# Performance work log

Hardware: AMD Instinct MI355X
Metric: run time of the kernel (lower is better)

The kernel has to match this reference:

```python
import jax, jax.numpy as jnp
import numpy as np

B = 2048       # batch
D_IN = 512     # input_size
D_MODEL = 1024 # hidden_size / d_model
ED = 2048      # d_inner = 2*d_model
N = 16         # d_state
K = 4          # d_conv
DT = 64        # dt_rank = ceil(d_model/16)
FLAT_H = ED * N
RMS_EPS = 1e-5


def setup_inputs() -> dict:
    key = jax.random.key(0)
    ks = jax.random.split(key, 12)
    rn = lambda k, shape, s: jax.random.normal(k, shape, jnp.float32) * s
    return {
        "x_t": rn(ks[0], (B, D_IN), 1.0),
        "flat_state": rn(ks[1], (B, FLAT_H + ED * (K - 1)), 0.1),
        "W_in_cell": rn(ks[2], (D_MODEL, D_IN), D_IN ** -0.5),
        "norm_w": jnp.ones((D_MODEL,), jnp.float32),
        "W_in": rn(ks[3], (2 * ED, D_MODEL), D_MODEL ** -0.5),
        "conv_w": rn(ks[4], (ED, K), K ** -0.5),  # depthwise conv weight (ED,1,K) squeezed
        "conv_b": rn(ks[5], (ED,), 0.02),
        "W_xproj": rn(ks[6], (DT + 2 * N, ED), ED ** -0.5),
        "W_dt": rn(ks[7], (ED, DT), DT ** -0.5),
        "b_dt": rn(ks[8], (ED,), 0.02),
        "A_log": jnp.log(jnp.broadcast_to(jnp.arange(1, N + 1, dtype=jnp.float32), (ED, N))),
        "D_param": jnp.ones((ED,), jnp.float32),
        "W_out": rn(ks[9], (D_MODEL, ED), ED ** -0.5),
    }


def _rmsnorm(x, w):
    return x * jax.lax.rsqrt(jnp.mean(x * x, axis=-1, keepdims=True) + RMS_EPS) * w


def reference(x_t, flat_state, W_in_cell, norm_w, W_in, conv_w, conv_b,
              W_xproj, W_dt, b_dt, A_log, D_param, W_out):
    # MambaCell.in_proj (bias=False)
    x = x_t @ W_in_cell.T                                  # (B, D_MODEL)
    # unpack flat recurrent state
    h = flat_state[:, :FLAT_H].reshape(B, ED, N)           # SSM state
    inputs = flat_state[:, FLAT_H:].reshape(B, ED, K - 1)  # conv cache

    residual = x
    xn = _rmsnorm(x, norm_w)

    # MambaBlock.step
    xz = xn @ W_in.T                                       # (B, 2*ED)
    x1, z = xz[:, :ED], xz[:, ED:]

    # depthwise causal conv, last output position only
    window = jnp.concatenate([inputs, x1[:, :, None]], axis=2)   # (B, ED, K)
    xc = jnp.einsum("bek,ek->be", window, conv_w) + conv_b
    xs = jax.nn.silu(xc)                                   # (B, ED)

    # selective SSM single step
    dbc = xs @ W_xproj.T                                   # (B, DT+2N)
    delta = jax.nn.softplus(dbc[:, :DT] @ W_dt.T + b_dt)   # (B, ED)
    Bm = dbc[:, DT:DT + N]                                 # (B, N)
    Cm = dbc[:, DT + N:]                                   # (B, N)
    A = -jnp.exp(A_log)                                    # (ED, N)
    dA = jnp.exp(delta[:, :, None] * A[None])              # (B, ED, N)
    dBx = delta[:, :, None] * Bm[:, None, :] * xs[:, :, None]
    h_new = dA * h + dBx                                   # (B, ED, N)
    y = jnp.einsum("ben,bn->be", h_new, Cm) + D_param * xs

    out = (y * jax.nn.silu(z)) @ W_out.T                   # (B, D_MODEL)
    y_t = out + residual                                   # residual connection in ResidualBlock.step

    inputs_new = jnp.concatenate([inputs[:, :, 1:], x1[:, :, None]], axis=2)
    flat_new = jax.lax.stop_gradient(
        jnp.concatenate([h_new.reshape(B, -1), inputs_new.reshape(B, -1)], axis=1))
    return y_t, flat_new
```

## Files before the change

### kernel.cpp

```cpp
#include <hip/hip_runtime.h>
#include <math.h>

#define B 2048
#define D_IN 512
#define D_MODEL 1024
#define ED 2048
#define NSTATE 16
#define KCONV 4
#define DTDIM 64
#define FLAT_H (ED * NSTATE)
#define ROW_STATE (FLAT_H + ED * (KCONV - 1))

typedef __attribute__((ext_vector_type(8))) short short8;
typedef __attribute__((ext_vector_type(4))) short short4v;
typedef __attribute__((ext_vector_type(4))) float f32x4;

__device__ __forceinline__ float sigmoidf_(float x) { return 1.f / (1.f + expf(-x)); }

__device__ __forceinline__ unsigned short f2bf(float f) {
  unsigned u = __float_as_uint(f);
  u += 0x7FFFu + ((u >> 16) & 1u);
  return (unsigned short)(u >> 16);
}
__device__ __forceinline__ float bf2f(unsigned short h) {
  return __uint_as_float((unsigned)h << 16);
}

template <int MODE>
__global__ __launch_bounds__(256) void gemm_nt_mfma(
    const float* __restrict__ A, const float* __restrict__ W,
    float* __restrict__ C, int M, int N, int K, int lda, int ldw, int ldc,
    const float* __restrict__ extra) {
  __shared__ short Ahi[4][128][8];
  __shared__ short Alo[4][128][8];
  __shared__ short Whi[4][128][8];
  __shared__ short Wlo[4][128][8];

  const int tid = threadIdx.x;
  const int lane = tid & 63;
  const int wave = tid >> 6;
  const int wr = wave >> 1;
  const int wc = wave & 1;
  const int m0 = blockIdx.y * 128;
  const int n0 = blockIdx.x * 128;
  const int kg = lane >> 4;
  const int lr = lane & 15;

  f32x4 acc[4][4] = {};

  for (int k0 = 0; k0 < K; k0 += 32) {
#pragma unroll
    for (int it = 0; it < 4; ++it) {
      const int flat = tid + it * 256;
      const int row = flat >> 3;
      const int kq = flat & 7;
      const int tkg = kq >> 1;
      const int j0 = (kq & 1) * 4;
      const float4 av = *(const float4*)(A + (size_t)(m0 + row) * lda + (k0 + kq * 4));
      const float4 wv = *(const float4*)(W + (size_t)(n0 + row) * ldw + (k0 + kq * 4));
      const float af[4] = {av.x, av.y, av.z, av.w};
      const float wf[4] = {wv.x, wv.y, wv.z, wv.w};
      short4v ah, al, wh, wl;
#pragma unroll
      for (int e = 0; e < 4; ++e) {
        const unsigned short h = f2bf(af[e]);
        ah[e] = (short)h;
        al[e] = (short)f2bf(af[e] - bf2f(h));
        const unsigned short hw = f2bf(wf[e]);
        wh[e] = (short)hw;
        wl[e] = (short)f2bf(wf[e] - bf2f(hw));
      }
      *(short4v*)&Ahi[tkg][row][j0] = ah;
      *(short4v*)&Alo[tkg][row][j0] = al;
      *(short4v*)&Whi[tkg][row][j0] = wh;
      *(short4v*)&Wlo[tkg][row][j0] = wl;
    }
    __syncthreads();

    short8 a_h[4], a_l[4], b_h[4], b_l[4];
#pragma unroll
    for (int i = 0; i < 4; ++i) {
      a_h[i] = *(const short8*)&Ahi[kg][wr * 64 + i * 16 + lr][0];
      a_l[i] = *(const short8*)&Alo[kg][wr * 64 + i * 16 + lr][0];
      b_h[i] = *(const short8*)&Whi[kg][wc * 64 + i * 16 + lr][0];
      b_l[i] = *(const short8*)&Wlo[kg][wc * 64 + i * 16 + lr][0];
    }
#pragma unroll
    for (int i = 0; i < 4; ++i)
#pragma unroll
      for (int j = 0; j < 4; ++j) {
        acc[i][j] = __builtin_amdgcn_mfma_f32_16x16x32_bf16(a_h[i], b_h[j], acc[i][j], 0, 0, 0);
        acc[i][j] = __builtin_amdgcn_mfma_f32_16x16x32_bf16(a_l[i], b_h[j], acc[i][j], 0, 0, 0);
        acc[i][j] = __builtin_amdgcn_mfma_f32_16x16x32_bf16(a_h[i], b_l[j], acc[i][j], 0, 0, 0);
      }
    __syncthreads();
  }

#pragma unroll
  for (int i = 0; i < 4; ++i) {
    const int gm = m0 + wr * 64 + i * 16 + kg * 4;
#pragma unroll
    for (int j = 0; j < 4; ++j) {
      const int gn = n0 + wc * 64 + j * 16 + lr;
#pragma unroll
      for (int r = 0; r < 4; ++r) {
        float v = acc[i][j][r];
        if (MODE == 1) {
          v += extra[gn];
          v = (v > 20.f) ? v : log1pf(expf(v));
        } else if (MODE == 2) {
          v += extra[(size_t)(gm + r) * ldc + gn];
        }
        C[(size_t)(gm + r) * ldc + gn] = v;
      }
    }
  }
}

__global__ __launch_bounds__(256) void gemm_nt_splitk(
    const float* __restrict__ A, const float* __restrict__ W,
    float* __restrict__ C, int M, int N, int K, int lda, int ldw, int ldc) {
  __shared__ float As[16][68];
  __shared__ float Ws[16][68];
  const int tid = threadIdx.x;
  const int tx = tid & 15;
  const int ty = tid >> 4;
  const int m0 = blockIdx.y * 64;
  const int n0 = blockIdx.x * 64;
  const int kchunk = K / gridDim.z;
  const int kbeg = blockIdx.z * kchunk;

  float acc[4][4] = {};
  const int lr = tid >> 4;
  const int lc = tid & 15;

  for (int k0 = kbeg; k0 < kbeg + kchunk; k0 += 16) {
#pragma unroll
    for (int i = 0; i < 4; i++) {
      const int r = lr + i * 16;
      const int gk = k0 + lc;
      As[lc][r] = A[(size_t)(m0 + r) * lda + gk];
      const int gn = n0 + r;
      Ws[lc][r] = (gn < N) ? W[(size_t)gn * ldw + gk] : 0.f;
    }
    __syncthreads();
#pragma unroll
    for (int k = 0; k < 16; k++) {
      float a[4], w[4];
#pragma unroll
      for (int i = 0; i < 4; i++) a[i] = As[k][ty * 4 + i];
#pragma unroll
      for (int j = 0; j < 4; j++) w[j] = Ws[k][tx * 4 + j];
#pragma unroll
      for (int i = 0; i < 4; i++)
#pragma unroll
        for (int j = 0; j < 4; j++) acc[i][j] += a[i] * w[j];
    }
    __syncthreads();
  }

#pragma unroll
  for (int i = 0; i < 4; i++) {
    const int gm = m0 + ty * 4 + i;
#pragma unroll
    for (int j = 0; j < 4; j++) {
      const int gn = n0 + tx * 4 + j;
      if (gn >= N) continue;
      atomicAdd(&C[(size_t)gm * ldc + gn], acc[i][j]);
    }
  }
}

__global__ __launch_bounds__(256) void rmsnorm_kernel(
    const float* __restrict__ x, const float* __restrict__ w,
    float* __restrict__ xn) {
  const int b = blockIdx.x;
  const float* xr = x + (size_t)b * D_MODEL;
  float ss = 0.f;
  for (int i = threadIdx.x; i < D_MODEL; i += 256) {
    float v = xr[i];
    ss += v * v;
  }
#pragma unroll
  for (int off = 32; off > 0; off >>= 1) ss += __shfl_down(ss, off, 64);
  __shared__ float red[4];
  if ((threadIdx.x & 63) == 0) red[threadIdx.x >> 6] = ss;
  __syncthreads();
  const float tot = red[0] + red[1] + red[2] + red[3];
  const float scale = rsqrtf(tot * (1.f / (float)D_MODEL) + 1e-5f);
  float* xnr = xn + (size_t)b * D_MODEL;
  for (int i = threadIdx.x; i < D_MODEL; i += 256) xnr[i] = xr[i] * scale * w[i];
}

__global__ __launch_bounds__(256) void conv_silu_kernel(
    const float* __restrict__ flat_state, const float* __restrict__ xz,
    const float* __restrict__ conv_w, const float* __restrict__ conv_b,
    float* __restrict__ xs, float* __restrict__ outFlat) {
  const int id = blockIdx.x * 256 + threadIdx.x;
  const int b = id >> 11;
  const int e = id & (ED - 1);
  const float* inp = flat_state + (size_t)b * ROW_STATE + FLAT_H + e * 3;
  const float i0 = inp[0], i1 = inp[1], i2 = inp[2];
  const float x1 = xz[(size_t)b * (2 * ED) + e];
  const float* cw = conv_w + e * 4;
  const float xc = i0 * cw[0] + i1 * cw[1] + i2 * cw[2] + x1 * cw[3] + conv_b[e];
  xs[(size_t)b * ED + e] = xc * sigmoidf_(xc);
  float* on = outFlat + (size_t)b * ROW_STATE + FLAT_H + e * 3;
  on[0] = i1;
  on[1] = i2;
  on[2] = x1;
}

__global__ __launch_bounds__(256) void state_kernel(
    const float* __restrict__ flat_state, const float* __restrict__ xz,
    const float* __restrict__ xs, const float* __restrict__ dbc,
    const float* __restrict__ delta, const float* __restrict__ A_log,
    const float* __restrict__ D_param, float* __restrict__ outFlat,
    float* __restrict__ yz) {
  const int id = blockIdx.x * 256 + threadIdx.x;
  const int b = id >> 11;
  const int e = id & (ED - 1);
  const float d = delta[(size_t)b * ED + e];
  const float xsv = xs[(size_t)b * ED + e];
  const float* hb = flat_state + (size_t)b * ROW_STATE + e * NSTATE;
  float* ho = outFlat + (size_t)b * ROW_STATE + e * NSTATE;
  const float* dbcb = dbc + (size_t)b * 96;
  const float* al = A_log + e * NSTATE;
  float y = 0.f;
#pragma unroll
  for (int n = 0; n < NSTATE; n++) {
    const float Aen = -expf(al[n]);
    const float dA = expf(d * Aen);
    const float hn = dA * hb[n] + d * dbcb[DTDIM + n] * xsv;
    ho[n] = hn;
    y += hn * dbcb[DTDIM + NSTATE + n];
  }
  y += D_param[e] * xsv;
  const float z = xz[(size_t)b * (2 * ED) + ED + e];
  yz[(size_t)b * ED + e] = y * (z * sigmoidf_(z));
}

extern "C" void kernel_launch(void* const* d_in, const int* in_sizes, int n_in,
                              void* d_out, int out_size, void* d_ws, size_t ws_size,
                              hipStream_t stream) {
  const float* x_t       = (const float*)d_in[0];
  const float* flat_state= (const float*)d_in[1];
  const float* W_in_cell = (const float*)d_in[2];
  const float* norm_w    = (const float*)d_in[3];
  const float* W_in      = (const float*)d_in[4];
  const float* conv_w    = (const float*)d_in[5];
  const float* conv_b    = (const float*)d_in[6];
  const float* W_xproj   = (const float*)d_in[7];
  const float* W_dt      = (const float*)d_in[8];
  const float* b_dt      = (const float*)d_in[9];
  const float* A_log     = (const float*)d_in[10];
  const float* D_param   = (const float*)d_in[11];
  const float* W_out     = (const float*)d_in[12];

  float* y_t_out = (float*)d_out;
  float* outFlat = (float*)d_out + (size_t)B * D_MODEL;

  float* ws = (float*)d_ws;
  float* x     = ws;
  float* xn    = x + (size_t)B * D_MODEL;
  float* xz    = xn + (size_t)B * D_MODEL;
  float* xs    = xz + (size_t)B * 2 * ED;
  float* dbc   = xs + (size_t)B * ED;
  float* delta = dbc + (size_t)B * 96;
  float* yz    = delta + (size_t)B * ED;

  dim3 blk(256);

  hipMemsetAsync(dbc, 0, (size_t)B * 96 * sizeof(float), stream);

  gemm_nt_mfma<0><<<dim3(D_MODEL / 128, B / 128), blk, 0, stream>>>(
      x_t, W_in_cell, x, B, D_MODEL, D_IN, D_IN, D_IN, D_MODEL, nullptr);
  rmsnorm_kernel<<<dim3(B), blk, 0, stream>>>(x, norm_w, xn);
  gemm_nt_mfma<0><<<dim3(2 * ED / 128, B / 128), blk, 0, stream>>>(
      xn, W_in, xz, B, 2 * ED, D_MODEL, D_MODEL, D_MODEL, 2 * ED, nullptr);
  conv_silu_kernel<<<dim3((B * ED) / 256), blk, 0, stream>>>(
      flat_state, xz, conv_w, conv_b, xs, outFlat);
  gemm_nt_splitk<<<dim3(2, B / 64, 4), blk, 0, stream>>>(
      xs, W_xproj, dbc, B, 96, ED, ED, ED, 96);
  gemm_nt_mfma<1><<<dim3(ED / 128, B / 128), blk, 0, stream>>>(
      dbc, W_dt, delta, B, ED, DTDIM, 96, DTDIM, ED, b_dt);
  state_kernel<<<dim3((B * ED) / 256), blk, 0, stream>>>(
      flat_state, xz, xs, dbc, delta, A_log, D_param, outFlat, yz);
  gemm_nt_mfma<2><<<dim3(D_MODEL / 128, B / 128), blk, 0, stream>>>(
      yz, W_out, y_t_out, B, D_MODEL, ED, ED, ED, D_MODEL, x);
}
```

Before: 1.010 ms.

## Coalesce state and conv kernels, precompute -exp(A_log), vectorize rmsnorm

The SSM state update now gives each thread four consecutive state entries, loaded and stored as float4 so the large flat_state read and write are coalesced. Partial y sums are combined with lane shuffles. The -exp(A_log) term is computed once by a small prep kernel instead of per element, and written into the workspace slot of xn, which is dead by then. The conv kernel runs one block per batch row and stages the conv cache in LDS so global reads and writes are coalesced. RMSNorm is vectorized with float4 and the x-projection split-K depth goes from 4 to 8, at the cost of one extra launch and more atomic adds.

```diff
diff --git a/kernel.cpp b/kernel.cpp
--- a/kernel.cpp
+++ b/kernel.cpp
@@ -175,12 +175,9 @@
     const float* __restrict__ x, const float* __restrict__ w,
     float* __restrict__ xn) {
   const int b = blockIdx.x;
-  const float* xr = x + (size_t)b * D_MODEL;
-  float ss = 0.f;
-  for (int i = threadIdx.x; i < D_MODEL; i += 256) {
-    float v = xr[i];
-    ss += v * v;
-  }
+  const int i4 = threadIdx.x * 4;
+  const float4 v = *(const float4*)(x + (size_t)b * D_MODEL + i4);
+  float ss = v.x * v.x + v.y * v.y + v.z * v.z + v.w * v.w;
 #pragma unroll
   for (int off = 32; off > 0; off >>= 1) ss += __shfl_down(ss, off, 64);
   __shared__ float red[4];
@@ -188,56 +185,103 @@
   __syncthreads();
   const float tot = red[0] + red[1] + red[2] + red[3];
   const float scale = rsqrtf(tot * (1.f / (float)D_MODEL) + 1e-5f);
-  float* xnr = xn + (size_t)b * D_MODEL;
-  for (int i = threadIdx.x; i < D_MODEL; i += 256) xnr[i] = xr[i] * scale * w[i];
+  const float4 wv = *(const float4*)(w + i4);
+  float4 o;
+  o.x = v.x * scale * wv.x;
+  o.y = v.y * scale * wv.y;
+  o.z = v.z * scale * wv.z;
+  o.w = v.w * scale * wv.w;
+  *(float4*)(xn + (size_t)b * D_MODEL + i4) = o;
+}
+
+__global__ __launch_bounds__(256) void prep_aneg(
+    const float* __restrict__ A_log, float* __restrict__ Aneg) {
+  const int i4 = (blockIdx.x * 256 + threadIdx.x) * 4;
+  const float4 v = *(const float4*)(A_log + i4);
+  float4 o;
+  o.x = -expf(v.x);
+  o.y = -expf(v.y);
+  o.z = -expf(v.z);
+  o.w = -expf(v.w);
+  *(float4*)(Aneg + i4) = o;
 }
 
 __global__ __launch_bounds__(256) void conv_silu_kernel(
     const float* __restrict__ flat_state, const float* __restrict__ xz,
     const float* __restrict__ conv_w, const float* __restrict__ conv_b,
     float* __restrict__ xs, float* __restrict__ outFlat) {
-  const int id = blockIdx.x * 256 + threadIdx.x;
-  const int b = id >> 11;
-  const int e = id & (ED - 1);
-  const float* inp = flat_state + (size_t)b * ROW_STATE + FLAT_H + e * 3;
-  const float i0 = inp[0], i1 = inp[1], i2 = inp[2];
-  const float x1 = xz[(size_t)b * (2 * ED) + e];
-  const float* cw = conv_w + e * 4;
-  const float xc = i0 * cw[0] + i1 * cw[1] + i2 * cw[2] + x1 * cw[3] + conv_b[e];
-  xs[(size_t)b * ED + e] = xc * sigmoidf_(xc);
-  float* on = outFlat + (size_t)b * ROW_STATE + FLAT_H + e * 3;
-  on[0] = i1;
-  on[1] = i2;
-  on[2] = x1;
+  const int b = blockIdx.x;
+  __shared__ float sin_[ED * 3];
+  __shared__ float sx1[ED];
+  const float* inRow = flat_state + (size_t)b * ROW_STATE + FLAT_H;
+  const float* x1Row = xz + (size_t)b * (2 * ED);
+#pragma unroll
+  for (int i = 0; i < 6; ++i) {
+    const int idx = (threadIdx.x + i * 256) * 4;
+    *(float4*)&sin_[idx] = *(const float4*)&inRow[idx];
+  }
+#pragma unroll
+  for (int i = 0; i < 2; ++i) {
+    const int idx = (threadIdx.x + i * 256) * 4;
+    *(float4*)&sx1[idx] = *(const float4*)&x1Row[idx];
+  }
+  __syncthreads();
+  float* xsRow = xs + (size_t)b * ED;
+#pragma unroll
+  for (int k = 0; k < 8; ++k) {
+    const int e = threadIdx.x + k * 256;
+    const float4 cw = *(const float4*)(conv_w + e * 4);
+    const float xc = sin_[e * 3] * cw.x + sin_[e * 3 + 1] * cw.y +
+                     sin_[e * 3 + 2] * cw.z + sx1[e] * cw.w + conv_b[e];
+    xsRow[e] = xc * sigmoidf_(xc);
+  }
+  float* on = outFlat + (size_t)b * ROW_STATE + FLAT_H;
+#pragma unroll
+  for (int k = 0; k < 24; ++k) {
+    const int i = threadIdx.x + k * 256;
+    const int q = i / 3;
+    const int r = i - q * 3;
+    on[i] = (r == 2) ? sx1[q] : sin_[i + 1];
+  }
 }
 
 __global__ __launch_bounds__(256) void state_kernel(
     const float* __restrict__ flat_state, const float* __restrict__ xz,
     const float* __restrict__ xs, const float* __restrict__ dbc,
-    const float* __restrict__ delta, const float* __restrict__ A_log,
+    const float* __restrict__ delta, const float* __restrict__ Aneg,
     const float* __restrict__ D_param, float* __restrict__ outFlat,
     float* __restrict__ yz) {
   const int id = blockIdx.x * 256 + threadIdx.x;
-  const int b = id >> 11;
-  const int e = id & (ED - 1);
+  const int f = id << 2;
+  const int b = f >> 15;
+  const int off = f & 32767;
+  const int e = off >> 4;
+  const int n0 = off & 15;
+
   const float d = delta[(size_t)b * ED + e];
   const float xsv = xs[(size_t)b * ED + e];
-  const float* hb = flat_state + (size_t)b * ROW_STATE + e * NSTATE;
-  float* ho = outFlat + (size_t)b * ROW_STATE + e * NSTATE;
+  const float dx = d * xsv;
+  const float4 h4 = *(const float4*)(flat_state + (size_t)b * ROW_STATE + off);
+  const float4 a4 = *(const float4*)(Aneg + off);
   const float* dbcb = dbc + (size_t)b * 96;
-  const float* al = A_log + e * NSTATE;
-  float y = 0.f;
-#pragma unroll
-  for (int n = 0; n < NSTATE; n++) {
-    const float Aen = -expf(al[n]);
-    const float dA = expf(d * Aen);
-    const float hn = dA * hb[n] + d * dbcb[DTDIM + n] * xsv;
-    ho[n] = hn;
-    y += hn * dbcb[DTDIM + NSTATE + n];
-  }
-  y += D_param[e] * xsv;
-  const float z = xz[(size_t)b * (2 * ED) + ED + e];
-  yz[(size_t)b * ED + e] = y * (z * sigmoidf_(z));
+  const float4 B4 = *(const float4*)(dbcb + DTDIM + n0);
+  const float4 C4 = *(const float4*)(dbcb + DTDIM + NSTATE + n0);
+
+  float4 hn;
+  hn.x = expf(d * a4.x) * h4.x + dx * B4.x;
+  hn.y = expf(d * a4.y) * h4.y + dx * B4.y;
+  hn.z = expf(d * a4.z) * h4.z + dx * B4.z;
+  hn.w = expf(d * a4.w) * h4.w + dx * B4.w;
+  *(float4*)(outFlat + (size_t)b * ROW_STATE + off) = hn;
+
+  float y = hn.x * C4.x + hn.y * C4.y + hn.z * C4.z + hn.w * C4.w;
+  y += __shfl_xor(y, 1, 64);
+  y += __shfl_xor(y, 2, 64);
+  if (n0 == 0) {
+    y += D_param[e] * xsv;
+    const float z = xz[(size_t)b * (2 * ED) + ED + e];
+    yz[(size_t)b * ED + e] = y * (z * sigmoidf_(z));
+  }
 }
 
 extern "C" void kernel_launch(void* const* d_in, const int* in_sizes, int n_in,
@@ -268,24 +312,26 @@
   float* dbc   = xs + (size_t)B * ED;
   float* delta = dbc + (size_t)B * 96;
   float* yz    = delta + (size_t)B * ED;
+  float* Aneg  = xn;
 
   dim3 blk(256);
 
-  hipMemsetAsync(dbc, 0, (size_t)B * 96 * sizeof(float), stream);
+  (void)hipMemsetAsync(dbc, 0, (size_t)B * 96 * sizeof(float), stream);
 
   gemm_nt_mfma<0><<<dim3(D_MODEL / 128, B / 128), blk, 0, stream>>>(
       x_t, W_in_cell, x, B, D_MODEL, D_IN, D_IN, D_IN, D_MODEL, nullptr);
   rmsnorm_kernel<<<dim3(B), blk, 0, stream>>>(x, norm_w, xn);
   gemm_nt_mfma<0><<<dim3(2 * ED / 128, B / 128), blk, 0, stream>>>(
       xn, W_in, xz, B, 2 * ED, D_MODEL, D_MODEL, D_MODEL, 2 * ED, nullptr);
-  conv_silu_kernel<<<dim3((B * ED) / 256), blk, 0, stream>>>(
+  prep_aneg<<<dim3(ED * NSTATE / 1024), blk, 0, stream>>>(A_log, Aneg);
+  conv_silu_kernel<<<dim3(B), blk, 0, stream>>>(
       flat_state, xz, conv_w, conv_b, xs, outFlat);
-  gemm_nt_splitk<<<dim3(2, B / 64, 4), blk, 0, stream>>>(
+  gemm_nt_splitk<<<dim3(2, B / 64, 8), blk, 0, stream>>>(
       xs, W_xproj, dbc, B, 96, ED, ED, ED, 96);
   gemm_nt_mfma<1><<<dim3(ED / 128, B / 128), blk, 0, stream>>>(
       dbc, W_dt, delta, B, ED, DTDIM, 96, DTDIM, ED, b_dt);
-  state_kernel<<<dim3((B * ED) / 256), blk, 0, stream>>>(
-      flat_state, xz, xs, dbc, delta, A_log, D_param, outFlat, yz);
+  state_kernel<<<dim3((size_t)B * FLAT_H / 1024), blk, 0, stream>>>(
+      flat_state, xz, xs, dbc, delta, Aneg, D_param, outFlat, yz);
   gemm_nt_mfma<2><<<dim3(D_MODEL / 128, B / 128), blk, 0, stream>>>(
       yz, W_out, y_t_out, B, D_MODEL, ED, ED, ED, D_MODEL, x);
 }
```

After: 909.7 us. 9.9% less time.
